# Kernel tuning notes

Hardware: AMD Instinct MI355X
Metric: run time of the kernel (lower is better)

The kernel has to match this reference:

```python
import jax, jax.numpy as jnp
import numpy as np

N = 100000
E = 1600000
N_IN = 512
N_H = 128


def setup_inputs() -> dict:
    key = jax.random.key(0)
    ks = jax.random.split(key, 8)
    x = jax.random.normal(ks[0], (N, N_IN), dtype=jnp.float32)
    src = jax.random.randint(ks[1], (E,), 0, N, dtype=jnp.int32)
    dst = jax.random.randint(ks[2], (E,), 0, N, dtype=jnp.int32)
    perm = jax.random.permutation(ks[3], N).astype(jnp.int32)
    # GraphConv params (in_feats=512 -> out_feats=128), xavier-ish scale
    W = jax.random.normal(ks[4], (N_IN, N_H), dtype=jnp.float32) / np.sqrt(N_IN)
    b = jnp.zeros((N_H,), dtype=jnp.float32)
    alpha = jnp.full((N_H,), 0.25, dtype=jnp.float32)  # PReLU(n_h) init
    mlp_W = jax.random.normal(ks[5], (N_H, N_H), dtype=jnp.float32) / np.sqrt(N_H)
    mlp_b = jnp.zeros((N_H,), dtype=jnp.float32)
    return {"x": x, "src": src, "dst": dst, "perm": perm, "W": W, "b": b,
            "alpha": alpha, "mlp_W": mlp_W, "mlp_b": mlp_b, "batch_train": 0}


def _degree_norm(idx, n):
    deg = jax.ops.segment_sum(jnp.ones_like(idx, dtype=jnp.float32), idx, num_segments=n)
    return jnp.clip(deg, 1.0, None) ** -0.5  # [n]


def _gcn_layer(x, src, dst, W, b, alpha):
    n = x.shape[0]
    norm_out = _degree_norm(src, n)  # src-side out-degree norm
    norm_in = _degree_norm(dst, n)   # dst-side in-degree norm
    # in_feats > out_feats: apply weight first (DGL GraphConv ordering)
    h = x @ W                                  # [N, n_h]
    h = h * norm_out[:, None]
    agg = jax.ops.segment_sum(h[src], dst, num_segments=n)  # SpMM copy_u/sum
    agg = agg * norm_in[:, None] + b
    return jnp.where(agg >= 0, agg, alpha * agg)  # PReLU(n_h)


def reference(x, src, dst, perm, W, b, alpha, mlp_W, mlp_b, batch_train):
    z1 = _gcn_layer(x, src, dst, W, b, alpha)          # clean encoder
    z2 = _gcn_layer(x[perm], src, dst, W, b, alpha)    # corrupted encoder
    z1 = z1 @ mlp_W + mlp_b
    z2 = z2 @ mlp_W + mlp_b
    logit = jnp.concatenate((z1.sum(1), z2.sum(1)), axis=0)  # [2N]
    return logit
```

## Files before the change

### kernel.cpp

```cpp
#include <hip/hip_runtime.h>


typedef __bf16 bf16x8 __attribute__((ext_vector_type(8)));
typedef float f32x4 __attribute__((ext_vector_type(4)));

#define PAD 48
#define NBMAX 256
#define EPB 4096

__device__ inline unsigned short f2bf(float f) {
  unsigned u = __float_as_uint(f);
  u += 0x7fffu + ((u >> 16) & 1u);
  return (unsigned short)(u >> 16);
}
__device__ inline float2 bfpair(unsigned u) {
  float2 r;
  r.x = __uint_as_float(u << 16);
  r.y = __uint_as_float(u & 0xffff0000u);
  return r;
}

__global__ __launch_bounds__(256) void k_bin(const int* __restrict__ src,
                                             const int* __restrict__ dst,
                                             int* __restrict__ gCntD,
                                             int* __restrict__ gCntS,
                                             int* __restrict__ dstbin,
                                             unsigned short* __restrict__ srcbin,
                                             int E, int NB, int CAP) {
  __shared__ int2 stage[EPB];
  __shared__ int cntD[NBMAX], cntS[NBMAX], baseD[NBMAX], baseS[NBMAX];
  const int tid = threadIdx.x;
  const int e0 = blockIdx.x * EPB;
  const int nloc = min(EPB, E - e0);

  for (int b = tid; b < NB; b += 256) { cntD[b] = 0; cntS[b] = 0; }
  __syncthreads();

#pragma unroll
  for (int it = 0; it < EPB / 256; ++it) {
    int i = it * 256 + tid;
    if (i < nloc) {
      int s = src[e0 + i];
      int d = dst[e0 + i];
      stage[i] = make_int2(s, d);
      atomicAdd(&cntD[d >> 9], 1);
      atomicAdd(&cntS[s >> 9], 1);
    }
  }
  __syncthreads();

  for (int b = tid; b < NB; b += 256) {
    baseD[b] = atomicAdd(&gCntD[b], cntD[b]);
    baseS[b] = atomicAdd(&gCntS[b], cntS[b]);
    cntD[b] = 0;
    cntS[b] = 0;
  }
  __syncthreads();

#pragma unroll
  for (int it = 0; it < EPB / 256; ++it) {
    int i = it * 256 + tid;
    if (i < nloc) {
      int2 sd = stage[i];
      int s = sd.x, d = sd.y;
      int bd = d >> 9;
      int p = atomicAdd(&cntD[bd], 1) + baseD[bd];
      if (p < CAP) dstbin[(size_t)bd * CAP + p] = (s << 9) | (d & 511);
      int bs = s >> 9;
      int q = atomicAdd(&cntS[bs], 1) + baseS[bs];
      if (q < CAP) srcbin[(size_t)bs * CAP + q] = (unsigned short)(s & 511);
    }
  }
}

__global__ __launch_bounds__(256) void k_csr(const int* __restrict__ gCntD,
                                             const int* __restrict__ dstbin,
                                             int* __restrict__ col,
                                             int* __restrict__ deg_d,
                                             float* __restrict__ norm_i,
                                             int N, int CAP) {
  __shared__ int cnt[512];
  const int b = blockIdx.x;
  const int tid = threadIdx.x;
  cnt[tid] = 0;
  cnt[tid + 256] = 0;
  __syncthreads();
  int cb = gCntD[b];
  if (cb > CAP) cb = CAP;
  const int* bin = dstbin + (size_t)b * CAP;
  for (int i = tid; i < cb; i += 256) {
    int rec = bin[i];
    int d9 = rec & 511;
    int s = rec >> 9;
    int pos = atomicAdd(&cnt[d9], 1);
    if (pos < PAD) col[((size_t)b * 512 + d9) * PAD + pos] = s;
  }
  __syncthreads();
  for (int t = tid; t < 512; t += 256) {
    int i = b * 512 + t;
    if (i < N) {
      int c = cnt[t];
      deg_d[i] = (c > PAD) ? PAD : c;
      norm_i[i] = rsqrtf((float)((c < 1) ? 1 : c));
    }
  }
}

__global__ __launch_bounds__(256) void k_shist(const int* __restrict__ gCntS,
                                               const unsigned short* __restrict__ srcbin,
                                               const int* __restrict__ perm,
                                               float* __restrict__ norm_o,
                                               int* __restrict__ inv,
                                               int N, int CAP) {
  __shared__ int hist[512];
  const int b = blockIdx.x;
  const int tid = threadIdx.x;
  hist[tid] = 0;
  hist[tid + 256] = 0;
  __syncthreads();
  int cb = gCntS[b];
  if (cb > CAP) cb = CAP;
  const unsigned short* bin = srcbin + (size_t)b * CAP;
  for (int i = tid; i < cb; i += 256) {
    atomicAdd(&hist[bin[i]], 1);
  }
  __syncthreads();
  for (int t = tid; t < 512; t += 256) {
    int i = b * 512 + t;
    if (i < N) {
      int h = hist[t];
      norm_o[i] = rsqrtf((float)((h < 1) ? 1 : h));
      inv[perm[i]] = i;
    }
  }
}

__global__ __launch_bounds__(256) void k_fill_dev(const int* __restrict__ src,
                                                  const int* __restrict__ dst,
                                                  int* __restrict__ deg_s,
                                                  int* __restrict__ cnt,
                                                  int* __restrict__ col, int E) {
  int t = blockIdx.x * 256 + threadIdx.x;
  int e0 = t * 4;
  if (e0 >= E) return;
  int e1 = (e0 + 4 < E) ? e0 + 4 : E;
  for (int e = e0; e < e1; e++) {
    int s = src[e], d = dst[e];
    atomicAdd(&deg_s[s], 1);
    int pos = atomicAdd(&cnt[d], 1);
    if (pos < PAD) col[(size_t)d * PAD + pos] = s;
  }
}

__global__ __launch_bounds__(256) void k_finish_dev(const int* __restrict__ deg_s,
                                                    const int* __restrict__ cnt,
                                                    const int* __restrict__ perm,
                                                    float* __restrict__ norm_o,
                                                    float* __restrict__ norm_i,
                                                    int* __restrict__ deg_d,
                                                    int* __restrict__ inv, int N) {
  int i = blockIdx.x * 256 + threadIdx.x;
  if (i >= N) return;
  int a = deg_s[i]; if (a < 1) a = 1;
  int b = cnt[i];
  deg_d[i] = (b > PAD) ? PAD : b;
  if (b < 1) b = 1;
  norm_o[i] = rsqrtf((float)a);
  norm_i[i] = rsqrtf((float)b);
  inv[perm[i]] = i;
}

__global__ __launch_bounds__(256) void k_castw(const float* __restrict__ W,
                                               unsigned short* __restrict__ WT) {
  int i = blockIdx.x * 256 + threadIdx.x;
  int k = i >> 7;
  int n = i & 127;
  WT[n * 512 + k] = f2bf(W[i]);
}

__global__ __launch_bounds__(256) void k_gemm(const float* __restrict__ X,
                                              const unsigned short* __restrict__ WT,
                                              const float* __restrict__ norm_o,
                                              const int* __restrict__ inv,
                                              unsigned short* __restrict__ HH, int M) {
  __shared__ __align__(16) unsigned short smem[8192];

  const int tid = threadIdx.x;
  const int wave = tid >> 6;
  const int lane = tid & 63;
  const int m = lane & 15;
  const int quad = lane >> 4;
  const int block_row = blockIdx.x * 64;

  const int arow = block_row + wave * 16 + m;
  const float* xrow = X + (size_t)((arow < M) ? arow : 0) * 512 + quad * 8;
  const unsigned short* wbase = WT + (size_t)m * 512 + quad * 8;

  f32x4 acc[8];
#pragma unroll
  for (int t = 0; t < 8; t++) acc[t] = (f32x4){0.f, 0.f, 0.f, 0.f};

#pragma unroll
  for (int ks = 0; ks < 16; ks++) {
    float4 va0 = *(const float4*)(xrow + ks * 32);
    float4 va1 = *(const float4*)(xrow + ks * 32 + 4);
    union { bf16x8 v; unsigned short us[8]; } au;
    au.us[0] = f2bf(va0.x); au.us[1] = f2bf(va0.y);
    au.us[2] = f2bf(va0.z); au.us[3] = f2bf(va0.w);
    au.us[4] = f2bf(va1.x); au.us[5] = f2bf(va1.y);
    au.us[6] = f2bf(va1.z); au.us[7] = f2bf(va1.w);
#pragma unroll
    for (int t = 0; t < 8; t++) {
      bf16x8 b = *(const bf16x8*)(wbase + (size_t)t * 16 * 512 + ks * 32);
      acc[t] = __builtin_amdgcn_mfma_f32_16x16x32_bf16(au.v, b, acc[t], 0, 0, 0);
    }
  }

  float no1[4], no2[4];
#pragma unroll
  for (int r = 0; r < 4; r++) {
    int rr = block_row + wave * 16 + quad * 4 + r;
    no1[r] = 0.f;
    no2[r] = 0.f;
    if (rr < M) {
      no1[r] = norm_o[rr];
      no2[r] = norm_o[inv[rr]];
    }
  }

#pragma unroll
  for (int t = 0; t < 8; t++) {
    int c = t * 16 + m;
#pragma unroll
    for (int r = 0; r < 4; r++) {
      int row = wave * 16 + quad * 4 + r;
      smem[row * 128 + c] = f2bf(acc[t][r] * no1[r]);
    }
  }
  __syncthreads();
#pragma unroll
  for (int it = 0; it < 4; it++) {
    int idx = tid + it * 256;
    int row = idx >> 4;
    int c8 = (idx & 15) * 8;
    int gr = block_row + row;
    if (gr < M)
      *(int4*)(HH + (size_t)gr * 256 + c8) = *(int4*)&smem[row * 128 + c8];
  }
  __syncthreads();

#pragma unroll
  for (int t = 0; t < 8; t++) {
    int c = t * 16 + m;
#pragma unroll
    for (int r = 0; r < 4; r++) {
      int row = wave * 16 + quad * 4 + r;
      smem[row * 128 + c] = f2bf(acc[t][r] * no2[r]);
    }
  }
  __syncthreads();
#pragma unroll
  for (int it = 0; it < 4; it++) {
    int idx = tid + it * 256;
    int row = idx >> 4;
    int c8 = (idx & 15) * 8;
    int gr = block_row + row;
    if (gr < M) {
      int q = inv[gr];
      *(int4*)(HH + (size_t)q * 256 + 128 + c8) = *(int4*)&smem[row * 128 + c8];
    }
  }
}

__global__ __launch_bounds__(128) void k_wsum(const float* __restrict__ mlpW,
                                              const float* __restrict__ mlpb,
                                              float* __restrict__ wsum,
                                              float* __restrict__ bsum) {
  __shared__ float sb[128];
  int k = threadIdx.x;
  float s = 0.f;
  for (int j = 0; j < 128; j++) s += mlpW[k * 128 + j];
  wsum[k] = s;
  sb[k] = mlpb[k];
  __syncthreads();
  for (int off = 64; off > 0; off >>= 1) {
    if (k < off) sb[k] += sb[k + off];
    __syncthreads();
  }
  if (k == 0) bsum[0] = sb[0];
}

__global__ __launch_bounds__(256) void k_agg(const unsigned short* __restrict__ HH,
                                             const int* __restrict__ deg_d,
                                             const int* __restrict__ col,
                                             const float* __restrict__ norm_i,
                                             const float* __restrict__ bias,
                                             const float* __restrict__ alpha,
                                             const float* __restrict__ wsum,
                                             const float* __restrict__ bsum,
                                             float* __restrict__ out, int N) {
  int wave = (blockIdx.x * 256 + threadIdx.x) >> 6;
  int lane = threadIdx.x & 63;
  if (wave >= N) return;
  const int g = lane >> 4;
  const int sl = lane & 15;

  int cl = deg_d[wave];
  const int* cbase = col + (size_t)wave * PAD;

  float a1[8], a2[8];
#pragma unroll
  for (int i = 0; i < 8; i++) { a1[i] = 0.f; a2[i] = 0.f; }

  for (int j0 = 0; j0 < cl; j0 += 4) {
    int j = j0 + g;
    int je = (j < cl) ? j : cl - 1;
    int s = cbase[je];
    float mk = (j < cl) ? 1.f : 0.f;
    const unsigned short* rp = HH + (size_t)s * 256 + sl * 8;
    int4 r1 = *(const int4*)rp;
    int4 r2 = *(const int4*)(rp + 128);
    const unsigned* u1 = (const unsigned*)&r1;
    const unsigned* u2 = (const unsigned*)&r2;
#pragma unroll
    for (int q = 0; q < 4; q++) {
      float2 v1 = bfpair(u1[q]);
      float2 v2 = bfpair(u2[q]);
      a1[2 * q]     = fmaf(v1.x, mk, a1[2 * q]);
      a1[2 * q + 1] = fmaf(v1.y, mk, a1[2 * q + 1]);
      a2[2 * q]     = fmaf(v2.x, mk, a2[2 * q]);
      a2[2 * q + 1] = fmaf(v2.y, mk, a2[2 * q + 1]);
    }
  }

#pragma unroll
  for (int i = 0; i < 8; i++) {
    a1[i] += __shfl_xor(a1[i], 16);
    a1[i] += __shfl_xor(a1[i], 32);
    a2[i] += __shfl_xor(a2[i], 16);
    a2[i] += __shfl_xor(a2[i], 32);
  }

  float ni = norm_i[wave];
  float4 bb0 = ((const float4*)bias)[sl * 2];
  float4 bb1 = ((const float4*)bias)[sl * 2 + 1];
  float4 al0 = ((const float4*)alpha)[sl * 2];
  float4 al1 = ((const float4*)alpha)[sl * 2 + 1];
  float4 ws0 = ((const float4*)wsum)[sl * 2];
  float4 ws1 = ((const float4*)wsum)[sl * 2 + 1];
  float bs = bsum[0];
  float bb[8] = {bb0.x, bb0.y, bb0.z, bb0.w, bb1.x, bb1.y, bb1.z, bb1.w};
  float al[8] = {al0.x, al0.y, al0.z, al0.w, al1.x, al1.y, al1.z, al1.w};
  float wsv[8] = {ws0.x, ws0.y, ws0.z, ws0.w, ws1.x, ws1.y, ws1.z, ws1.w};

  float p1 = 0.f, p2 = 0.f;
#pragma unroll
  for (int i = 0; i < 8; i++) {
    float g1 = a1[i] * ni + bb[i];
    float g2 = a2[i] * ni + bb[i];
    g1 = (g1 >= 0.f) ? g1 : al[i] * g1;
    g2 = (g2 >= 0.f) ? g2 : al[i] * g2;
    p1 = fmaf(g1, wsv[i], p1);
    p2 = fmaf(g2, wsv[i], p2);
  }
#pragma unroll
  for (int off = 8; off > 0; off >>= 1) {
    p1 += __shfl_down(p1, off);
    p2 += __shfl_down(p2, off);
  }
  if (lane == 0) {
    out[wave] = p1 + bs;
    out[N + wave] = p2 + bs;
  }
}


extern "C" void kernel_launch(void* const* d_in, const int* in_sizes, int n_in,
                              void* d_out, int out_size, void* d_ws, size_t ws_size,
                              hipStream_t stream) {
  const float* x = (const float*)d_in[0];
  const int* src = (const int*)d_in[1];
  const int* dst = (const int*)d_in[2];
  const int* perm = (const int*)d_in[3];
  const float* W = (const float*)d_in[4];
  const float* bias = (const float*)d_in[5];
  const float* alpha = (const float*)d_in[6];
  const float* mlpW = (const float*)d_in[7];
  const float* mlpb = (const float*)d_in[8];

  const int E = in_sizes[1];
  const int N = in_sizes[3];
  float* out = (float*)d_out;

  char* ws = (char*)d_ws;
  size_t off = 0;
  auto alloc = [&](size_t bytes) -> void* {
    void* p = ws + off;
    off = (off + bytes + 255) & ~(size_t)255;
    return p;
  };

  unsigned short* HH = (unsigned short*)alloc((size_t)N * 256 * sizeof(unsigned short));
  int* col = (int*)alloc((size_t)N * PAD * sizeof(int));
  unsigned short* WT = (unsigned short*)alloc(512 * 128 * sizeof(unsigned short));
  float* norm_o = (float*)alloc((size_t)N * sizeof(float));
  float* norm_i = (float*)alloc((size_t)N * sizeof(float));
  int* inv = (int*)alloc((size_t)N * sizeof(int));
  int* deg_d = (int*)alloc((size_t)N * sizeof(int));
  float* wsum = (float*)alloc(512);
  float* bsum = (float*)alloc(256);
  size_t common = off;

  const int NB = (N + 511) >> 9;
  const int meanB = (NB > 0) ? E / NB : 0;
  const int CAP = ((meanB * 5) / 4 + 1023) & ~1023;

  size_t need_binned = common + (size_t)NB * CAP * sizeof(int) +
                       (size_t)NB * CAP * sizeof(unsigned short) +
                       2 * (size_t)NBMAX * sizeof(int) + 4096;
  bool binned = (NB <= NBMAX) && ((ws_size == 0) || (ws_size >= need_binned));

  const int nbN = (N + 255) / 256;
  const int nbE4 = ((E + 3) / 4 + 255) / 256;

  k_castw<<<512 * 128 / 256, 256, 0, stream>>>(W, WT);
  k_wsum<<<1, 128, 0, stream>>>(mlpW, mlpb, wsum, bsum);

  if (binned) {
    int* dstbin = (int*)alloc((size_t)NB * CAP * sizeof(int));
    unsigned short* srcbin = (unsigned short*)alloc((size_t)NB * CAP * sizeof(unsigned short));
    int* gCntD = (int*)alloc((size_t)NBMAX * sizeof(int));
    int* gCntS = (int*)alloc((size_t)NBMAX * sizeof(int));
    hipMemsetAsync(gCntD, 0, (size_t)NBMAX * sizeof(int), stream);
    hipMemsetAsync(gCntS, 0, (size_t)NBMAX * sizeof(int), stream);
    const int nbBin = (E + EPB - 1) / EPB;
    k_bin<<<nbBin, 256, 0, stream>>>(src, dst, gCntD, gCntS, dstbin, srcbin,
                                     E, NB, CAP);
    k_csr<<<NB, 256, 0, stream>>>(gCntD, dstbin, col, deg_d, norm_i, N, CAP);
    k_shist<<<NB, 256, 0, stream>>>(gCntS, srcbin, perm, norm_o, inv, N, CAP);
  } else {
    int* deg_s = (int*)alloc((size_t)N * sizeof(int));
    int* cnt = (int*)alloc((size_t)N * sizeof(int));
    hipMemsetAsync(deg_s, 0, (size_t)N * sizeof(int), stream);
    hipMemsetAsync(cnt, 0, (size_t)N * sizeof(int), stream);
    k_fill_dev<<<nbE4, 256, 0, stream>>>(src, dst, deg_s, cnt, col, E);
    k_finish_dev<<<nbN, 256, 0, stream>>>(deg_s, cnt, perm, norm_o, norm_i,
                                          deg_d, inv, N);
  }

  k_gemm<<<(N + 63) / 64, 256, 0, stream>>>(x, WT, norm_o, inv, HH, N);
  k_agg<<<(N + 3) / 4, 256, 0, stream>>>(HH, deg_d, col, norm_i,
                                         bias, alpha, wsum, bsum, out, N);
}
```

Measured before the change: 565.2 us.

## Double-buffer GEMM operand tiles in LDS via async global_load_lds

The X@W GEMM kernel now stages the A (fp32 X) and B (bf16 WT) k-tiles into LDS with global_load_lds, double-buffered so the next k-slice loads while MFMAs run on the current one. Previously each wave read X and W straight from global memory with no reuse of W across waves. The A tile uses an XOR swizzle to avoid LDS bank conflicts. The cost is a barrier per k-step and 32KB of LDS, which may lower occupancy. Float-to-bf16 conversion now uses the native cast instead of the manual rounding routine.

Result: faster. 514.2 us (-9.0%).

```diff
diff --git a/kernel.cpp b/kernel.cpp
--- a/kernel.cpp
+++ b/kernel.cpp
@@ -18,6 +18,12 @@
   r.x = __uint_as_float(u << 16);
   r.y = __uint_as_float(u & 0xffff0000u);
   return r;
+}
+
+__device__ __forceinline__ void gld16(const void* g, void* l) {
+  __builtin_amdgcn_global_load_lds(
+      (const __attribute__((address_space(1))) void*)g,
+      (__attribute__((address_space(3))) void*)l, 16, 0, 0);
 }
 
 __global__ __launch_bounds__(256) void k_bin(const int* __restrict__ src,
@@ -183,7 +189,10 @@
                                               const float* __restrict__ norm_o,
                                               const int* __restrict__ inv,
                                               unsigned short* __restrict__ HH, int M) {
-  __shared__ __align__(16) unsigned short smem[8192];
+  __shared__ __align__(16) unsigned char lds_raw[32768];
+  float* Asf = (float*)lds_raw;
+  unsigned short* Bsh = (unsigned short*)(lds_raw + 16384);
+  unsigned short* smem = (unsigned short*)lds_raw;
 
   const int tid = threadIdx.x;
   const int wave = tid >> 6;
@@ -192,39 +201,70 @@
   const int quad = lane >> 4;
   const int block_row = blockIdx.x * 64;
 
-  const int arow = block_row + wave * 16 + m;
-  const float* xrow = X + (size_t)((arow < M) ? arow : 0) * 512 + quad * 8;
-  const unsigned short* wbase = WT + (size_t)m * 512 + quad * 8;
-
   f32x4 acc[8];
 #pragma unroll
   for (int t = 0; t < 8; t++) acc[t] = (f32x4){0.f, 0.f, 0.f, 0.f};
 
-#pragma unroll
-  for (int ks = 0; ks < 16; ks++) {
-    float4 va0 = *(const float4*)(xrow + ks * 32);
-    float4 va1 = *(const float4*)(xrow + ks * 32 + 4);
-    union { bf16x8 v; unsigned short us[8]; } au;
-    au.us[0] = f2bf(va0.x); au.us[1] = f2bf(va0.y);
-    au.us[2] = f2bf(va0.z); au.us[3] = f2bf(va0.w);
-    au.us[4] = f2bf(va1.x); au.us[5] = f2bf(va1.y);
-    au.us[6] = f2bf(va1.z); au.us[7] = f2bf(va1.w);
-#pragma unroll
-    for (int t = 0; t < 8; t++) {
-      bf16x8 b = *(const bf16x8*)(wbase + (size_t)t * 16 * 512 + ks * 32);
+  const int ar0 = tid >> 3, as0 = (tid & 7) ^ (ar0 & 7);
+  const int g1 = 256 + tid;
+  const int ar1 = g1 >> 3, as1 = (g1 & 7) ^ (ar1 & 7);
+  int gra0 = block_row + ar0; if (gra0 >= M) gra0 = M - 1;
+  int gra1 = block_row + ar1; if (gra1 >= M) gra1 = M - 1;
+  const float* srcA0 = X + (size_t)gra0 * 512 + as0 * 4;
+  const float* srcA1 = X + (size_t)gra1 * 512 + as1 * 4;
+  const int bn0 = tid >> 2, bs0 = tid & 3;
+  const int bn1 = g1 >> 2, bs1 = g1 & 3;
+  const unsigned short* srcB0 = WT + (size_t)bn0 * 512 + bs0 * 8;
+  const unsigned short* srcB1 = WT + (size_t)bn1 * 512 + bs1 * 8;
+
+  auto stage = [&](int buf, int kt) {
+    const int k0 = kt * 32;
+    float* la = Asf + buf * 2048;
+    unsigned short* lb = Bsh + buf * 4096;
+    gld16(srcA0 + k0, la + tid * 4);
+    gld16(srcA1 + k0, la + g1 * 4);
+    gld16(srcB0 + k0, lb + tid * 8);
+    gld16(srcB1 + k0, lb + g1 * 8);
+  };
+
+  stage(0, 0);
+  __syncthreads();
+
+  const int r = wave * 16 + m;
+  const int sl0 = ((quad * 2) ^ (r & 7)) * 4;
+  const int sl1 = ((quad * 2 + 1) ^ (r & 7)) * 4;
+
+  int cur = 0;
+  for (int kt = 0; kt < 16; ++kt) {
+    if (kt < 15) stage(cur ^ 1, kt + 1);
+    const float* Ab = Asf + cur * 2048;
+    const unsigned short* Bb = Bsh + cur * 4096;
+    f32x4 a0 = *(const f32x4*)(Ab + r * 32 + sl0);
+    f32x4 a1 = *(const f32x4*)(Ab + r * 32 + sl1);
+    union { bf16x8 v; __bf16 h[8]; } au;
+#pragma unroll
+    for (int j = 0; j < 4; ++j) {
+      au.h[j] = (__bf16)a0[j];
+      au.h[4 + j] = (__bf16)a1[j];
+    }
+#pragma unroll
+    for (int t = 0; t < 8; ++t) {
+      bf16x8 b = *(const bf16x8*)(Bb + (t * 16 + m) * 32 + quad * 8);
       acc[t] = __builtin_amdgcn_mfma_f32_16x16x32_bf16(au.v, b, acc[t], 0, 0, 0);
     }
+    __syncthreads();
+    cur ^= 1;
   }
 
   float no1[4], no2[4];
 #pragma unroll
-  for (int r = 0; r < 4; r++) {
-    int rr = block_row + wave * 16 + quad * 4 + r;
-    no1[r] = 0.f;
-    no2[r] = 0.f;
+  for (int rr4 = 0; rr4 < 4; rr4++) {
+    int rr = block_row + wave * 16 + quad * 4 + rr4;
+    no1[rr4] = 0.f;
+    no2[rr4] = 0.f;
     if (rr < M) {
-      no1[r] = norm_o[rr];
-      no2[r] = norm_o[inv[rr]];
+      no1[rr4] = norm_o[rr];
+      no2[rr4] = norm_o[inv[rr]];
     }
   }
 
@@ -232,9 +272,9 @@
   for (int t = 0; t < 8; t++) {
     int c = t * 16 + m;
 #pragma unroll
-    for (int r = 0; r < 4; r++) {
-      int row = wave * 16 + quad * 4 + r;
-      smem[row * 128 + c] = f2bf(acc[t][r] * no1[r]);
+    for (int rr4 = 0; rr4 < 4; rr4++) {
+      int row = wave * 16 + quad * 4 + rr4;
+      smem[row * 128 + c] = f2bf(acc[t][rr4] * no1[rr4]);
     }
   }
   __syncthreads();
@@ -253,9 +293,9 @@
   for (int t = 0; t < 8; t++) {
     int c = t * 16 + m;
 #pragma unroll
-    for (int r = 0; r < 4; r++) {
-      int row = wave * 16 + quad * 4 + r;
-      smem[row * 128 + c] = f2bf(acc[t][r] * no2[r]);
+    for (int rr4 = 0; rr4 < 4; rr4++) {
+      int row = wave * 16 + quad * 4 + rr4;
+      smem[row * 128 + c] = f2bf(acc[t][rr4] * no2[rr4]);
     }
   }
   __syncthreads();
```
